# Kernel optimization log

Measured on AMD Instinct MI355X. Metric: run time of the kernel, lower is better.

## Reference

```python
import jax, jax.numpy as jnp
import numpy as np

NUM_HEADS = 32
NUM_KV_HEADS = 8
HEAD_DIM = 64


def rotate_half(x):
    x1, x2 = jnp.split(x, 2, axis=-1)
    return jnp.concatenate((-x2, x1), axis=-1)


def setup_inputs() -> dict:
    key = jax.random.key(0)
    ks = jax.random.split(key, 7)
    B, S, H = 2, 2048, 2048
    hidden_states = jax.random.normal(ks[0], (B, S, H), dtype=jnp.float32)
    # RoPE angles: build realistic cos/sin from inv_freq for positions 0..S-1
    inv_freq = 1.0 / (10000.0 ** (np.arange(0, HEAD_DIM, 2, dtype=np.float32) / HEAD_DIM))
    t = np.arange(S, dtype=np.float32)
    freqs = np.outer(t, inv_freq)  # [S, HEAD_DIM/2]
    emb = np.concatenate([freqs, freqs], axis=-1)  # [S, HEAD_DIM]
    cos = jnp.broadcast_to(jnp.cos(emb)[None], (B, S, HEAD_DIM)).astype(jnp.float32)
    sin = jnp.broadcast_to(jnp.sin(emb)[None], (B, S, HEAD_DIM)).astype(jnp.float32)
    scale = 1.0 / np.sqrt(H)
    Wq = jax.random.normal(ks[1], (NUM_HEADS * HEAD_DIM, H), dtype=jnp.float32) * scale
    Wk = jax.random.normal(ks[2], (NUM_KV_HEADS * HEAD_DIM, H), dtype=jnp.float32) * scale
    Wv = jax.random.normal(ks[3], (NUM_KV_HEADS * HEAD_DIM, H), dtype=jnp.float32) * scale
    Wo = jax.random.normal(ks[4], (H, H), dtype=jnp.float32) * scale
    return {"hidden_states": hidden_states, "cos": cos, "sin": sin,
            "Wq": Wq, "Wk": Wk, "Wv": Wv, "Wo": Wo}


def reference(hidden_states, cos, sin, Wq, Wk, Wv, Wo):
    B, S, H = hidden_states.shape
    hd = HEAD_DIM
    # QKV projections (torch Linear: y = x @ W.T)
    q = jnp.einsum('bsi,oi->bso', hidden_states, Wq).reshape(B, S, NUM_HEADS, hd).transpose(0, 2, 1, 3)
    k = jnp.einsum('bsi,oi->bso', hidden_states, Wk).reshape(B, S, NUM_KV_HEADS, hd).transpose(0, 2, 1, 3)
    v = jnp.einsum('bsi,oi->bso', hidden_states, Wv).reshape(B, S, NUM_KV_HEADS, hd).transpose(0, 2, 1, 3)
    # RoPE: cos/sin [B,S,hd] -> [B,1,S,hd] broadcast over heads
    c = cos[:, None, :, :]
    s = sin[:, None, :, :]
    q = q * c + rotate_half(q) * s
    k = k * c + rotate_half(k) * s
    # GQA: repeat kv heads to match query heads
    groups = NUM_HEADS // NUM_KV_HEADS
    k = jnp.repeat(k, groups, axis=1)
    v = jnp.repeat(v, groups, axis=1)
    scaling = hd ** -0.5
    scores = jnp.einsum('bhqd,bhkd->bhqk', q, k) * scaling
    causal = jnp.tril(jnp.ones((S, S), dtype=bool))
    scores = jnp.where(causal, scores, jnp.finfo(scores.dtype).min)
    attn = jax.nn.softmax(scores, axis=-1)
    y = jnp.einsum('bhqk,bhkd->bhqd', attn, v)
    y = y.transpose(0, 2, 1, 3).reshape(B, S, H)
    return jnp.einsum('bsi,oi->bso', y, Wo)
```

## Files before the change

kernel.cpp:

```cpp
#include <hip/hip_runtime.h>

typedef __bf16 bf16_t;
typedef bf16_t bf16x8 __attribute__((ext_vector_type(8)));
typedef bf16_t bf16x4 __attribute__((ext_vector_type(4)));
typedef float f32x4 __attribute__((ext_vector_type(4)));
typedef float f32x16 __attribute__((ext_vector_type(16)));

#define MFMA16(a, b, c) __builtin_amdgcn_mfma_f32_16x16x32_bf16(a, b, c, 0, 0, 0)
#define MFMA32(a, b, c) __builtin_amdgcn_mfma_f32_32x32x16_bf16(a, b, c, 0, 0, 0)

#define GLOAD16(gsrc, ldst)                                            \
  __builtin_amdgcn_global_load_lds(                                    \
      (const __attribute__((address_space(1))) void*)(gsrc),           \
      (__attribute__((address_space(3))) void*)(ldst), 16, 0, 0)

constexpr int B_ = 2, S_ = 2048, H_ = 2048, NH = 32, NKV = 8, HD = 64;
constexpr int NQKV = NH * HD + 2 * NKV * HD;
constexpr int M_ROWS = B_ * S_;
constexpr float QSCALE = 0.125f * 1.4426950408889634f;

__global__ __launch_bounds__(256) void cvt_kernel(const float* __restrict__ in,
                                                  bf16_t* __restrict__ out, int n8) {
  int i = blockIdx.x * 256 + threadIdx.x;
  if (i >= n8) return;
  const float4* p = (const float4*)(in + (size_t)i * 8);
  float4 a = p[0], b = p[1];
  bf16x8 o;
  o[0] = (bf16_t)a.x; o[1] = (bf16_t)a.y; o[2] = (bf16_t)a.z; o[3] = (bf16_t)a.w;
  o[4] = (bf16_t)b.x; o[5] = (bf16_t)b.y; o[6] = (bf16_t)b.z; o[7] = (bf16_t)b.w;
  *(bf16x8*)(out + (size_t)i * 8) = o;
}

__global__ __launch_bounds__(256) void cvt3_kernel(const float* __restrict__ s0,
                                                   const float* __restrict__ s1,
                                                   const float* __restrict__ s2,
                                                   bf16_t* __restrict__ out) {
  int i = blockIdx.x * 256 + threadIdx.x;
  const float* src;
  long off;
  if (i < 524288) { src = s0; off = i; }
  else if (i < 655360) { src = s1; off = i - 524288; }
  else { src = s2; off = i - 655360; }
  const float4* p = (const float4*)(src + off * 8);
  float4 a = p[0], b = p[1];
  bf16x8 o;
  o[0] = (bf16_t)a.x; o[1] = (bf16_t)a.y; o[2] = (bf16_t)a.z; o[3] = (bf16_t)a.w;
  o[4] = (bf16_t)b.x; o[5] = (bf16_t)b.y; o[6] = (bf16_t)b.z; o[7] = (bf16_t)b.w;
  *(bf16x8*)(out + (size_t)i * 8) = o;
}

template <bool OUT_BF16>
__global__ __launch_bounds__(256) void gemm_bt(const bf16_t* __restrict__ A,
                                               const bf16_t* __restrict__ Bm,
                                               float* __restrict__ Cf,
                                               bf16_t* __restrict__ Cb,
                                               int M, int N, int K) {
  __shared__ __align__(16) bf16_t As[2][128 * 32];
  __shared__ __align__(16) bf16_t Bs[2][128 * 32];
  const int t = threadIdx.x;
  const int lane = t & 63, w = t >> 6;
  const int l15 = lane & 15, l4 = lane >> 4;
  const int wm = w >> 1, wn = w & 1;
  const long Ar0 = (long)blockIdx.y * 128;
  const long Br0 = (long)blockIdx.x * 128;
  const int nt = K >> 5;

  const int scol = ((lane & 3) ^ ((lane >> 3) & 3)) * 8;
  const int srow = lane >> 2;
  auto stage = [&](int kt, int buf) {
#pragma unroll
    for (int c = 0; c < 2; ++c) {
      const int i = w * 2 + c;
      const bf16_t* gA = A + (Ar0 + i * 16 + srow) * (long)K + kt * 32 + scol;
      const bf16_t* gB = Bm + (Br0 + i * 16 + srow) * (long)K + kt * 32 + scol;
      GLOAD16(gA, &As[buf][i * 512]);
      GLOAD16(gB, &Bs[buf][i * 512]);
    }
  };

  f32x4 acc[4][4] = {};
  stage(0, 0);
  __syncthreads();
  int cur = 0;
  const int rsw = l4 ^ ((l15 >> 1) & 3);
  for (int kt = 0; kt < nt; ++kt) {
    if (kt + 1 < nt) stage(kt + 1, cur ^ 1);
    bf16x8 af[4], bfr[4];
#pragma unroll
    for (int mf = 0; mf < 4; ++mf)
      af[mf] = *(const bf16x8*)&As[cur][(wm * 64 + mf * 16 + l15) * 32 + rsw * 8];
#pragma unroll
    for (int nf = 0; nf < 4; ++nf)
      bfr[nf] = *(const bf16x8*)&Bs[cur][(wn * 64 + nf * 16 + l15) * 32 + rsw * 8];
#pragma unroll
    for (int mf = 0; mf < 4; ++mf)
#pragma unroll
      for (int nf = 0; nf < 4; ++nf)
        acc[mf][nf] = MFMA16(af[mf], bfr[nf], acc[mf][nf]);
    __syncthreads();
    cur ^= 1;
  }
#pragma unroll
  for (int mf = 0; mf < 4; ++mf)
#pragma unroll
    for (int nf = 0; nf < 4; ++nf)
#pragma unroll
      for (int r = 0; r < 4; ++r) {
        long row = Ar0 + wm * 64 + mf * 16 + l4 * 4 + r;
        long col = Br0 + wn * 64 + nf * 16 + l15;
        float v = acc[mf][nf][r];
        if (OUT_BF16)
          Cb[row * N + col] = (bf16_t)v;
        else
          Cf[row * N + col] = v;
      }
}

__global__ __launch_bounds__(256) void rope_kernel(bf16_t* __restrict__ qkv,
                                                   const float* __restrict__ cosb,
                                                   const float* __restrict__ sinb) {
  const int head = blockIdx.y;
  const int i = blockIdx.x * 256 + threadIdx.x;
  const long bs = i >> 2;
  const int d0 = (i & 3) * 8;
  const long base = bs * NQKV + (head < 32 ? head * 64 : 2048 + (head - 32) * 64) + d0;
  const float scl = head < 32 ? QSCALE : 1.0f;
  bf16x8 x1 = *(bf16x8*)(qkv + base);
  bf16x8 x2 = *(bf16x8*)(qkv + base + 32);
  const float4* cp = (const float4*)(cosb + bs * 64 + d0);
  const float4* sp = (const float4*)(sinb + bs * 64 + d0);
  const float4 c0 = cp[0], c1 = cp[1];
  const float4 s0 = sp[0], s1 = sp[1];
  const float cc[8] = {c0.x, c0.y, c0.z, c0.w, c1.x, c1.y, c1.z, c1.w};
  const float ss[8] = {s0.x, s0.y, s0.z, s0.w, s1.x, s1.y, s1.z, s1.w};
  bf16x8 y1, y2;
#pragma unroll
  for (int e = 0; e < 8; ++e) {
    const float f1 = (float)x1[e], f2 = (float)x2[e];
    y1[e] = (bf16_t)((f1 * cc[e] - f2 * ss[e]) * scl);
    y2[e] = (bf16_t)((f2 * cc[e] + f1 * ss[e]) * scl);
  }
  *(bf16x8*)(qkv + base) = y1;
  *(bf16x8*)(qkv + base + 32) = y2;
}

__global__ __launch_bounds__(256) void v_transpose(const bf16_t* __restrict__ qkv,
                                                   bf16_t* __restrict__ vT) {
  __shared__ __align__(16) bf16_t lds[64 * 64];
  const int b = blockIdx.z, kvh = blockIdx.y, s0 = blockIdx.x * 64;
  const int t = threadIdx.x;
  auto key = [](int s) { return (((s & 7) ^ ((s >> 3) & 7)) << 3); };
  const int si = t >> 3, j8 = (t & 7) * 8;
  const bf16_t* src = qkv + ((long)(b * S_ + s0 + si)) * NQKV + 2560 + kvh * 64 + j8;
  *(bf16x8*)&lds[si * 64 + (j8 ^ key(si))] = *(const bf16x8*)src;
  *(bf16x8*)&lds[(si + 32) * 64 + (j8 ^ key(si + 32))] =
      *(const bf16x8*)(src + 32L * NQKV);
  __syncthreads();
  const int d = t >> 2, sg = (t & 3) * 16;
  bf16x8 o0, o1;
#pragma unroll
  for (int e = 0; e < 8; ++e) {
    o0[e] = lds[(sg + e) * 64 + (d ^ key(sg + e))];
    o1[e] = lds[(sg + 8 + e) * 64 + (d ^ key(sg + 8 + e))];
  }
  bf16_t* dst = vT + ((long)(b * NKV + kvh) * 64 + d) * S_ + s0 + sg;
  *(bf16x8*)dst = o0;
  *(bf16x8*)(dst + 8) = o1;
}

__device__ __forceinline__ unsigned pkbf16(float lo, float hi) {
  union { bf16_t h[2]; unsigned u; } x;
  x.h[0] = (bf16_t)lo;
  x.h[1] = (bf16_t)hi;
  return x.u;
}

__global__ __launch_bounds__(128) void attn32_kernel(const bf16_t* __restrict__ qkv,
                                                     const bf16_t* __restrict__ vT,
                                                     bf16_t* __restrict__ y) {
  const int h = blockIdx.y;
  const int b = blockIdx.z;
  const int kvh = h >> 2;
  const int t = threadIdx.x, lane = t & 63, w = t >> 6;
  const int l31 = lane & 31, hd = lane >> 5;
  const long bS = (long)b * S_;

  __shared__ __align__(16) bf16_t Klds[2][64 * 64];
  __shared__ __align__(16) bf16_t Vlds[2][64 * 64];

  const bf16_t* kbase = qkv + bS * NQKV + NH * HD + kvh * 64;
  const bf16_t* vbase = vT + ((long)(b * NKV + kvh)) * 64 * S_;

  const int row0 = t >> 3;
  const int slot = t & 7;
  const int wslot8 = ((slot ^ (row0 & 7)) << 3);
  bf16x8 kreg[4], vreg[4];

  auto ldG = [&](int kv0) {
#pragma unroll
    for (int c = 0; c < 4; ++c) {
      kreg[c] = *(const bf16x8*)(kbase + (long)(kv0 + row0 + 16 * c) * NQKV + slot * 8);
      vreg[c] = *(const bf16x8*)(vbase + (long)(row0 + 16 * c) * S_ + kv0 + slot * 8);
    }
  };
  auto wrLDS = [&](int buf) {
#pragma unroll
    for (int c = 0; c < 4; ++c) {
      *(bf16x8*)&Klds[buf][(row0 + 16 * c) * 64 + wslot8] = kreg[c];
      *(bf16x8*)&Vlds[buf][(row0 + 16 * c) * 64 + wslot8] = vreg[c];
    }
  };

  for (int half = 0; half < 2; ++half) {
    const int qt = half ? (int)blockIdx.x : 31 - (int)blockIdx.x;
    const int q0w = qt * 64 + w * 32;
    const int myq = q0w + l31;
    const int NT = qt + 1;

    const bf16_t* qp = qkv + (bS + myq) * NQKV + h * 64 + hd * 8;
    bf16x8 qf[4];
#pragma unroll
    for (int ks = 0; ks < 4; ++ks) qf[ks] = *(const bf16x8*)(qp + ks * 16);

    f32x16 yac[2] = {};
    float m = -1e30f, l = 0.f;

    ldG(0);
    wrLDS(0);
    __syncthreads();

    for (int kt = 0; kt < NT; ++kt) {
      const int buf = kt & 1;
      const int kv0 = kt * 64;
      if (kt + 1 < NT) ldG(kv0 + 64);

      f32x16 sac[2] = {};
      __builtin_amdgcn_s_setprio(1);
#pragma unroll
      for (int ks = 0; ks < 4; ++ks)
#pragma unroll
        for (int kb = 0; kb < 2; ++kb) {
          const int row = kb * 32 + l31;
          const bf16x8 kf =
              *(const bf16x8*)&Klds[buf][row * 64 + (((2 * ks + hd) ^ (row & 7)) << 3)];
          sac[kb] = MFMA32(kf, qf[ks], sac[kb]);
        }
      __builtin_amdgcn_s_setprio(0);
      if (kv0 + 63 > q0w) {
#pragma unroll
        for (int kb = 0; kb < 2; ++kb)
#pragma unroll
          for (int r = 0; r < 16; ++r) {
            const int kv = kv0 + kb * 32 + (r & 3) + 8 * (r >> 2) + 4 * hd;
            if (kv > myq) sac[kb][r] = -3.0e38f;
          }
      }
      float pm4[8], sm4[8];
#pragma unroll
      for (int g = 0; g < 8; ++g) {
        const int kb = g >> 2, r = (g & 3) * 4;
        pm4[g] = fmaxf(fmaxf(sac[kb][r], sac[kb][r + 1]),
                       fmaxf(sac[kb][r + 2], sac[kb][r + 3]));
      }
      float pm = fmaxf(fmaxf(fmaxf(pm4[0], pm4[1]), fmaxf(pm4[2], pm4[3])),
                       fmaxf(fmaxf(pm4[4], pm4[5]), fmaxf(pm4[6], pm4[7])));
      pm = fmaxf(pm, __shfl_xor(pm, 32, 64));
      if (!__all(pm <= m + 8.f)) {
        const float mnew = fmaxf(m, pm);
        const float sc = __builtin_amdgcn_exp2f(m - mnew);
        l *= sc;
        yac[0] *= sc;
        yac[1] *= sc;
        m = mnew;
      }
#pragma unroll
      for (int kb = 0; kb < 2; ++kb)
#pragma unroll
        for (int r = 0; r < 16; ++r)
          sac[kb][r] = __builtin_amdgcn_exp2f(sac[kb][r] - m);
#pragma unroll
      for (int g = 0; g < 8; ++g) {
        const int kb = g >> 2, r = (g & 3) * 4;
        sm4[g] = (sac[kb][r] + sac[kb][r + 1]) + (sac[kb][r + 2] + sac[kb][r + 3]);
      }
      l += ((sm4[0] + sm4[1]) + (sm4[2] + sm4[3])) +
           ((sm4[4] + sm4[5]) + (sm4[6] + sm4[7]));
#pragma unroll
      for (int ks = 0; ks < 4; ++ks) {
        const int kb = ks >> 1;
        const int Bv = 8 * (ks & 1);
        unsigned a0 = pkbf16(sac[kb][Bv + 0], sac[kb][Bv + 1]);
        unsigned b0 = pkbf16(sac[kb][Bv + 4], sac[kb][Bv + 5]);
        unsigned a1 = pkbf16(sac[kb][Bv + 2], sac[kb][Bv + 3]);
        unsigned b1 = pkbf16(sac[kb][Bv + 6], sac[kb][Bv + 7]);
        asm("v_permlane32_swap_b32 %0, %1" : "+v"(a0), "+v"(b0));
        asm("v_permlane32_swap_b32 %0, %1" : "+v"(a1), "+v"(b1));
        union { unsigned u[4]; bf16x8 v; } pu;
        pu.u[0] = a0; pu.u[1] = a1; pu.u[2] = b0; pu.u[3] = b1;
        __builtin_amdgcn_s_setprio(1);
#pragma unroll
        for (int db = 0; db < 2; ++db) {
          const int row = db * 32 + l31;
          const bf16x8 vf =
              *(const bf16x8*)&Vlds[buf][row * 64 + (((2 * ks + hd) ^ (row & 7)) << 3)];
          yac[db] = MFMA32(vf, pu.v, yac[db]);
        }
        __builtin_amdgcn_s_setprio(0);
      }

      if (kt + 1 < NT) wrLDS(buf ^ 1);
      __syncthreads();
    }

    l += __shfl_xor(l, 32, 64);
    const float inv = __builtin_amdgcn_rcpf(l);
    bf16_t* yp = y + (bS + myq) * (long)H_ + h * 64;
#pragma unroll
    for (int db = 0; db < 2; ++db)
#pragma unroll
      for (int g = 0; g < 4; ++g) {
        bf16x4 o;
        o[0] = (bf16_t)(yac[db][4 * g + 0] * inv);
        o[1] = (bf16_t)(yac[db][4 * g + 1] * inv);
        o[2] = (bf16_t)(yac[db][4 * g + 2] * inv);
        o[3] = (bf16_t)(yac[db][4 * g + 3] * inv);
        *(bf16x4*)(yp + db * 32 + 8 * g + 4 * hd) = o;
      }
  }
}

extern "C" void kernel_launch(void* const* d_in, const int* in_sizes, int n_in,
                              void* d_out, int out_size, void* d_ws, size_t ws_size,
                              hipStream_t stream) {
  const float* hs = (const float*)d_in[0];
  const float* cosb = (const float*)d_in[1];
  const float* sinb = (const float*)d_in[2];
  const float* Wq = (const float*)d_in[3];
  const float* Wk = (const float*)d_in[4];
  const float* Wv = (const float*)d_in[5];
  const float* Wo = (const float*)d_in[6];
  float* out = (float*)d_out;

  char* ws = (char*)d_ws;
  bf16_t* hsb  = (bf16_t*)(ws);
  bf16_t* wqkv = (bf16_t*)(ws + 16777216);
  bf16_t* wo   = (bf16_t*)(ws + 29360128);
  bf16_t* qkv  = (bf16_t*)(ws + 37748736);
  bf16_t* vT   = (bf16_t*)(ws + 62914560);
  bf16_t* yb   = (bf16_t*)(ws + 67108864);

  cvt_kernel<<<4096, 256, 0, stream>>>(hs, hsb, 1048576);
  cvt3_kernel<<<3072, 256, 0, stream>>>(Wq, Wk, Wv, wqkv);
  cvt_kernel<<<2048, 256, 0, stream>>>(Wo, wo, 524288);

  gemm_bt<true><<<dim3(24, 32), 256, 0, stream>>>(hsb, wqkv, nullptr, qkv,
                                                  M_ROWS, NQKV, H_);
  rope_kernel<<<dim3(64, 40), 256, 0, stream>>>(qkv, cosb, sinb);
  v_transpose<<<dim3(32, 8, 2), 256, 0, stream>>>(qkv, vT);
  attn32_kernel<<<dim3(16, 32, 2), 128, 0, stream>>>(qkv, vT, yb);
  gemm_bt<false><<<dim3(16, 32), 256, 0, stream>>>(yb, wo, out, nullptr,
                                                   M_ROWS, H_, H_);
}
```

Baseline: 221.6 us.

## Load V fragments directly from global and drop paired-tile blocks in attention

The attention kernel now reads V operands straight from global memory (the transposed V buffer) into registers per lane instead of staging them through LDS. This halves shared memory use and removes the V LDS stores and loads. The grid is doubled so each block handles one query tile rather than a heavy/light pair, with heaviest tiles launched first. The tradeoff is uncoalesced, redundant global V reads per wave (both waves load the same V) and reliance on cache, plus less static load balancing within a block.

```diff
diff --git a/kernel.cpp b/kernel.cpp
--- a/kernel.cpp
+++ b/kernel.cpp
@@ -178,6 +178,7 @@
 __global__ __launch_bounds__(128) void attn32_kernel(const bf16_t* __restrict__ qkv,
                                                      const bf16_t* __restrict__ vT,
                                                      bf16_t* __restrict__ y) {
+  const int qt = 31 - (int)blockIdx.x;
   const int h = blockIdx.y;
   const int b = blockIdx.z;
   const int kvh = h >> 2;
@@ -186,147 +187,154 @@
   const long bS = (long)b * S_;
 
   __shared__ __align__(16) bf16_t Klds[2][64 * 64];
-  __shared__ __align__(16) bf16_t Vlds[2][64 * 64];
 
   const bf16_t* kbase = qkv + bS * NQKV + NH * HD + kvh * 64;
   const bf16_t* vbase = vT + ((long)(b * NKV + kvh)) * 64 * S_;
-
-  const int row0 = t >> 3;
-  const int slot = t & 7;
+  const bf16_t* vlane = vbase + (long)l31 * S_ + hd * 8;
+
+  const int row0 = t >> 3, slot = t & 7;
   const int wslot8 = ((slot ^ (row0 & 7)) << 3);
-  bf16x8 kreg[4], vreg[4];
-
-  auto ldG = [&](int kv0) {
+  const bf16_t* kp[4];
+#pragma unroll
+  for (int c = 0; c < 4; ++c)
+    kp[c] = kbase + (long)(row0 + 16 * c) * NQKV + slot * 8;
+  bf16x8 kreg[4];
+
+  auto ldG = [&]() {
 #pragma unroll
     for (int c = 0; c < 4; ++c) {
-      kreg[c] = *(const bf16x8*)(kbase + (long)(kv0 + row0 + 16 * c) * NQKV + slot * 8);
-      vreg[c] = *(const bf16x8*)(vbase + (long)(row0 + 16 * c) * S_ + kv0 + slot * 8);
+      kreg[c] = *(const bf16x8*)kp[c];
+      kp[c] += 64L * NQKV;
     }
   };
   auto wrLDS = [&](int buf) {
 #pragma unroll
-    for (int c = 0; c < 4; ++c) {
+    for (int c = 0; c < 4; ++c)
       *(bf16x8*)&Klds[buf][(row0 + 16 * c) * 64 + wslot8] = kreg[c];
-      *(bf16x8*)&Vlds[buf][(row0 + 16 * c) * 64 + wslot8] = vreg[c];
-    }
   };
 
-  for (int half = 0; half < 2; ++half) {
-    const int qt = half ? (int)blockIdx.x : 31 - (int)blockIdx.x;
-    const int q0w = qt * 64 + w * 32;
-    const int myq = q0w + l31;
-    const int NT = qt + 1;
-
-    const bf16_t* qp = qkv + (bS + myq) * NQKV + h * 64 + hd * 8;
-    bf16x8 qf[4];
-#pragma unroll
-    for (int ks = 0; ks < 4; ++ks) qf[ks] = *(const bf16x8*)(qp + ks * 16);
-
-    f32x16 yac[2] = {};
-    float m = -1e30f, l = 0.f;
-
-    ldG(0);
-    wrLDS(0);
+  const int q0w = qt * 64 + w * 32;
+  const int myq = q0w + l31;
+  const int NT = qt + 1;
+
+  const bf16_t* qp = qkv + (bS + myq) * NQKV + h * 64 + hd * 8;
+  bf16x8 qf[4];
+#pragma unroll
+  for (int ks = 0; ks < 4; ++ks) qf[ks] = *(const bf16x8*)(qp + ks * 16);
+
+  f32x16 yac[2] = {};
+  float m = -1e30f, l = 0.f;
+
+  ldG();
+  wrLDS(0);
+  __syncthreads();
+
+  for (int kt = 0; kt < NT; ++kt) {
+    const int buf = kt & 1;
+    const int kv0 = kt * 64;
+    if (kt + 1 < NT) ldG();
+
+    const bf16_t* Kb = &Klds[buf][0];
+
+    f32x16 sac[2] = {};
+    __builtin_amdgcn_s_setprio(1);
+#pragma unroll
+    for (int ks = 0; ks < 4; ++ks)
+#pragma unroll
+      for (int kb = 0; kb < 2; ++kb) {
+        const int row = kb * 32 + l31;
+        const bf16x8 kf =
+            *(const bf16x8*)&Kb[row * 64 + (((2 * ks + hd) ^ (row & 7)) << 3)];
+        sac[kb] = MFMA32(kf, qf[ks], sac[kb]);
+      }
+    __builtin_amdgcn_s_setprio(0);
+
+    bf16x8 vld[4][2];
+    {
+      const bf16_t* pv0 = vlane + kv0;
+#pragma unroll
+      for (int ks = 0; ks < 4; ++ks) {
+        vld[ks][0] = *(const bf16x8*)(pv0 + ks * 16);
+        vld[ks][1] = *(const bf16x8*)(pv0 + 32L * S_ + ks * 16);
+      }
+    }
+
+    if (kv0 + 63 > q0w) {
+#pragma unroll
+      for (int kb = 0; kb < 2; ++kb)
+#pragma unroll
+        for (int r = 0; r < 16; ++r) {
+          const int kv = kv0 + kb * 32 + (r & 3) + 8 * (r >> 2) + 4 * hd;
+          if (kv > myq) sac[kb][r] = -3.0e38f;
+        }
+    }
+    float pm4[8], sm4[8];
+#pragma unroll
+    for (int g = 0; g < 8; ++g) {
+      const int kb = g >> 2, r = (g & 3) * 4;
+      pm4[g] = fmaxf(fmaxf(sac[kb][r], sac[kb][r + 1]),
+                     fmaxf(sac[kb][r + 2], sac[kb][r + 3]));
+    }
+    float pm = fmaxf(fmaxf(fmaxf(pm4[0], pm4[1]), fmaxf(pm4[2], pm4[3])),
+                     fmaxf(fmaxf(pm4[4], pm4[5]), fmaxf(pm4[6], pm4[7])));
+    pm = fmaxf(pm, __shfl_xor(pm, 32, 64));
+    if (!__all(pm <= m + 8.f)) {
+      const float mnew = fmaxf(m, pm);
+      const float sc = __builtin_amdgcn_exp2f(m - mnew);
+      l *= sc;
+      yac[0] *= sc;
+      yac[1] *= sc;
+      m = mnew;
+    }
+#pragma unroll
+    for (int kb = 0; kb < 2; ++kb)
+#pragma unroll
+      for (int r = 0; r < 16; ++r)
+        sac[kb][r] = __builtin_amdgcn_exp2f(sac[kb][r] - m);
+#pragma unroll
+    for (int g = 0; g < 8; ++g) {
+      const int kb = g >> 2, r = (g & 3) * 4;
+      sm4[g] = (sac[kb][r] + sac[kb][r + 1]) + (sac[kb][r + 2] + sac[kb][r + 3]);
+    }
+    l += ((sm4[0] + sm4[1]) + (sm4[2] + sm4[3])) +
+         ((sm4[4] + sm4[5]) + (sm4[6] + sm4[7]));
+#pragma unroll
+    for (int ks = 0; ks < 4; ++ks) {
+      const int kb = ks >> 1;
+      const int Bv = 8 * (ks & 1);
+      unsigned a0 = pkbf16(sac[kb][Bv + 0], sac[kb][Bv + 1]);
+      unsigned b0 = pkbf16(sac[kb][Bv + 4], sac[kb][Bv + 5]);
+      unsigned a1 = pkbf16(sac[kb][Bv + 2], sac[kb][Bv + 3]);
+      unsigned b1 = pkbf16(sac[kb][Bv + 6], sac[kb][Bv + 7]);
+      asm("v_permlane32_swap_b32 %0, %1" : "+v"(a0), "+v"(b0));
+      asm("v_permlane32_swap_b32 %0, %1" : "+v"(a1), "+v"(b1));
+      union { unsigned u[4]; bf16x8 v; } pu;
+      pu.u[0] = a0; pu.u[1] = a1; pu.u[2] = b0; pu.u[3] = b1;
+      __builtin_amdgcn_s_setprio(1);
+#pragma unroll
+      for (int db = 0; db < 2; ++db)
+        yac[db] = MFMA32(vld[ks][db], pu.v, yac[db]);
+      __builtin_amdgcn_s_setprio(0);
+    }
+
+    if (kt + 1 < NT) wrLDS(buf ^ 1);
     __syncthreads();
-
-    for (int kt = 0; kt < NT; ++kt) {
-      const int buf = kt & 1;
-      const int kv0 = kt * 64;
-      if (kt + 1 < NT) ldG(kv0 + 64);
-
-      f32x16 sac[2] = {};
-      __builtin_amdgcn_s_setprio(1);
-#pragma unroll
-      for (int ks = 0; ks < 4; ++ks)
-#pragma unroll
-        for (int kb = 0; kb < 2; ++kb) {
-          const int row = kb * 32 + l31;
-          const bf16x8 kf =
-              *(const bf16x8*)&Klds[buf][row * 64 + (((2 * ks + hd) ^ (row & 7)) << 3)];
-          sac[kb] = MFMA32(kf, qf[ks], sac[kb]);
-        }
-      __builtin_amdgcn_s_setprio(0);
-      if (kv0 + 63 > q0w) {
-#pragma unroll
-        for (int kb = 0; kb < 2; ++kb)
-#pragma unroll
-          for (int r = 0; r < 16; ++r) {
-            const int kv = kv0 + kb * 32 + (r & 3) + 8 * (r >> 2) + 4 * hd;
-            if (kv > myq) sac[kb][r] = -3.0e38f;
-          }
-      }
-      float pm4[8], sm4[8];
-#pragma unroll
-      for (int g = 0; g < 8; ++g) {
-        const int kb = g >> 2, r = (g & 3) * 4;
-        pm4[g] = fmaxf(fmaxf(sac[kb][r], sac[kb][r + 1]),
-                       fmaxf(sac[kb][r + 2], sac[kb][r + 3]));
-      }
-      float pm = fmaxf(fmaxf(fmaxf(pm4[0], pm4[1]), fmaxf(pm4[2], pm4[3])),
-                       fmaxf(fmaxf(pm4[4], pm4[5]), fmaxf(pm4[6], pm4[7])));
-      pm = fmaxf(pm, __shfl_xor(pm, 32, 64));
-      if (!__all(pm <= m + 8.f)) {
-        const float mnew = fmaxf(m, pm);
-        const float sc = __builtin_amdgcn_exp2f(m - mnew);
-        l *= sc;
-        yac[0] *= sc;
-        yac[1] *= sc;
-        m = mnew;
-      }
-#pragma unroll
-      for (int kb = 0; kb < 2; ++kb)
-#pragma unroll
-        for (int r = 0; r < 16; ++r)
-          sac[kb][r] = __builtin_amdgcn_exp2f(sac[kb][r] - m);
-#pragma unroll
-      for (int g = 0; g < 8; ++g) {
-        const int kb = g >> 2, r = (g & 3) * 4;
-        sm4[g] = (sac[kb][r] + sac[kb][r + 1]) + (sac[kb][r + 2] + sac[kb][r + 3]);
-      }
-      l += ((sm4[0] + sm4[1]) + (sm4[2] + sm4[3])) +
-           ((sm4[4] + sm4[5]) + (sm4[6] + sm4[7]));
-#pragma unroll
-      for (int ks = 0; ks < 4; ++ks) {
-        const int kb = ks >> 1;
-        const int Bv = 8 * (ks & 1);
-        unsigned a0 = pkbf16(sac[kb][Bv + 0], sac[kb][Bv + 1]);
-        unsigned b0 = pkbf16(sac[kb][Bv + 4], sac[kb][Bv + 5]);
-        unsigned a1 = pkbf16(sac[kb][Bv + 2], sac[kb][Bv + 3]);
-        unsigned b1 = pkbf16(sac[kb][Bv + 6], sac[kb][Bv + 7]);
-        asm("v_permlane32_swap_b32 %0, %1" : "+v"(a0), "+v"(b0));
-        asm("v_permlane32_swap_b32 %0, %1" : "+v"(a1), "+v"(b1));
-        union { unsigned u[4]; bf16x8 v; } pu;
-        pu.u[0] = a0; pu.u[1] = a1; pu.u[2] = b0; pu.u[3] = b1;
-        __builtin_amdgcn_s_setprio(1);
-#pragma unroll
-        for (int db = 0; db < 2; ++db) {
-          const int row = db * 32 + l31;
-          const bf16x8 vf =
-              *(const bf16x8*)&Vlds[buf][row * 64 + (((2 * ks + hd) ^ (row & 7)) << 3)];
-          yac[db] = MFMA32(vf, pu.v, yac[db]);
-        }
-        __builtin_amdgcn_s_setprio(0);
-      }
-
-      if (kt + 1 < NT) wrLDS(buf ^ 1);
-      __syncthreads();
-    }
-
-    l += __shfl_xor(l, 32, 64);
-    const float inv = __builtin_amdgcn_rcpf(l);
-    bf16_t* yp = y + (bS + myq) * (long)H_ + h * 64;
-#pragma unroll
-    for (int db = 0; db < 2; ++db)
-#pragma unroll
-      for (int g = 0; g < 4; ++g) {
-        bf16x4 o;
-        o[0] = (bf16_t)(yac[db][4 * g + 0] * inv);
-        o[1] = (bf16_t)(yac[db][4 * g + 1] * inv);
-        o[2] = (bf16_t)(yac[db][4 * g + 2] * inv);
-        o[3] = (bf16_t)(yac[db][4 * g + 3] * inv);
-        *(bf16x4*)(yp + db * 32 + 8 * g + 4 * hd) = o;
-      }
   }
+
+  l += __shfl_xor(l, 32, 64);
+  const float inv = __builtin_amdgcn_rcpf(l);
+  bf16_t* yp = y + (bS + myq) * (long)H_ + h * 64;
+#pragma unroll
+  for (int db = 0; db < 2; ++db)
+#pragma unroll
+    for (int g = 0; g < 4; ++g) {
+      bf16x4 o;
+      o[0] = (bf16_t)(yac[db][4 * g + 0] * inv);
+      o[1] = (bf16_t)(yac[db][4 * g + 1] * inv);
+      o[2] = (bf16_t)(yac[db][4 * g + 2] * inv);
+      o[3] = (bf16_t)(yac[db][4 * g + 3] * inv);
+      *(bf16x4*)(yp + db * 32 + 8 * g + 4 * hd) = o;
+    }
 }
 
 extern "C" void kernel_launch(void* const* d_in, const int* in_sizes, int n_in,
@@ -357,7 +365,7 @@
                                                   M_ROWS, NQKV, H_);
   rope_kernel<<<dim3(64, 40), 256, 0, stream>>>(qkv, cosb, sinb);
   v_transpose<<<dim3(32, 8, 2), 256, 0, stream>>>(qkv, vT);
-  attn32_kernel<<<dim3(16, 32, 2), 128, 0, stream>>>(qkv, vT, yb);
+  attn32_kernel<<<dim3(32, 32, 2), 128, 0, stream>>>(qkv, vT, yb);
   gemm_bt<false><<<dim3(16, 32), 256, 0, stream>>>(yb, wo, out, nullptr,
                                                    M_ROWS, H_, H_);
 }
```

New measurement: 288.2 us. 1.3x slower.

## Share K/V tiles across the four GQA query heads in one attention block

Applied to the files above, without the earlier changes.

The attention kernel now launches 512 blocks of 512 threads, where each block handles one query tile for all four query heads that share a KV head. The K/V tiles staged in LDS are therefore reused by four heads instead of being loaded once per head. This replaces the earlier two-half loop that paired a long and a short causal tile within one block. Each thread now loads one K and one V vector per tile instead of four. The larger blocks and the launch bound asking for 4 blocks per CU may raise register pressure, and the causal work imbalance between blocks now depends on how the hardware schedules them.

```diff
diff --git a/kernel.cpp b/kernel.cpp
--- a/kernel.cpp
+++ b/kernel.cpp
@@ -175,14 +175,17 @@
   return x.u;
 }
 
-__global__ __launch_bounds__(128) void attn32_kernel(const bf16_t* __restrict__ qkv,
-                                                     const bf16_t* __restrict__ vT,
-                                                     bf16_t* __restrict__ y) {
-  const int h = blockIdx.y;
-  const int b = blockIdx.z;
-  const int kvh = h >> 2;
+__global__ __launch_bounds__(512, 4) void attn32_kernel(const bf16_t* __restrict__ qkv,
+                                                        const bf16_t* __restrict__ vT,
+                                                        bf16_t* __restrict__ y) {
+  const int bx = blockIdx.x;
+  const int p = (bx >> 1) & 15;
+  const int qt = (bx & 1) ? p : 31 - p;
+  const int kvh = (bx >> 5) & 7;
+  const int b = bx >> 8;
   const int t = threadIdx.x, lane = t & 63, w = t >> 6;
   const int l31 = lane & 31, hd = lane >> 5;
+  const int h = kvh * 4 + (w >> 1);
   const long bS = (long)b * S_;
 
   __shared__ __align__(16) bf16_t Klds[2][64 * 64];
@@ -191,142 +194,139 @@
   const bf16_t* kbase = qkv + bS * NQKV + NH * HD + kvh * 64;
   const bf16_t* vbase = vT + ((long)(b * NKV + kvh)) * 64 * S_;
 
-  const int row0 = t >> 3;
-  const int slot = t & 7;
+  const int row0 = t >> 3, slot = t & 7;
   const int wslot8 = ((slot ^ (row0 & 7)) << 3);
-  bf16x8 kreg[4], vreg[4];
-
-  auto ldG = [&](int kv0) {
-#pragma unroll
-    for (int c = 0; c < 4; ++c) {
-      kreg[c] = *(const bf16x8*)(kbase + (long)(kv0 + row0 + 16 * c) * NQKV + slot * 8);
-      vreg[c] = *(const bf16x8*)(vbase + (long)(row0 + 16 * c) * S_ + kv0 + slot * 8);
-    }
+  const bf16_t* kp = kbase + (long)row0 * NQKV + slot * 8;
+  const bf16_t* vp = vbase + (long)row0 * S_ + slot * 8;
+  bf16x8 kreg, vreg;
+
+  auto ldG = [&]() {
+    kreg = *(const bf16x8*)kp;
+    vreg = *(const bf16x8*)vp;
+    kp += 64L * NQKV;
+    vp += 64;
   };
   auto wrLDS = [&](int buf) {
-#pragma unroll
-    for (int c = 0; c < 4; ++c) {
-      *(bf16x8*)&Klds[buf][(row0 + 16 * c) * 64 + wslot8] = kreg[c];
-      *(bf16x8*)&Vlds[buf][(row0 + 16 * c) * 64 + wslot8] = vreg[c];
-    }
+    *(bf16x8*)&Klds[buf][row0 * 64 + wslot8] = kreg;
+    *(bf16x8*)&Vlds[buf][row0 * 64 + wslot8] = vreg;
   };
 
-  for (int half = 0; half < 2; ++half) {
-    const int qt = half ? (int)blockIdx.x : 31 - (int)blockIdx.x;
-    const int q0w = qt * 64 + w * 32;
-    const int myq = q0w + l31;
-    const int NT = qt + 1;
-
-    const bf16_t* qp = qkv + (bS + myq) * NQKV + h * 64 + hd * 8;
-    bf16x8 qf[4];
-#pragma unroll
-    for (int ks = 0; ks < 4; ++ks) qf[ks] = *(const bf16x8*)(qp + ks * 16);
-
-    f32x16 yac[2] = {};
-    float m = -1e30f, l = 0.f;
-
-    ldG(0);
-    wrLDS(0);
+  const int q0w = qt * 64 + (w & 1) * 32;
+  const int myq = q0w + l31;
+  const int NT = qt + 1;
+
+  const bf16_t* qp = qkv + (bS + myq) * NQKV + h * 64 + hd * 8;
+  bf16x8 qf[4];
+#pragma unroll
+  for (int ks = 0; ks < 4; ++ks) qf[ks] = *(const bf16x8*)(qp + ks * 16);
+
+  f32x16 yac[2] = {};
+  float m = -1e30f, l = 0.f;
+
+  ldG();
+  wrLDS(0);
+  __syncthreads();
+
+  for (int kt = 0; kt < NT; ++kt) {
+    const int buf = kt & 1;
+    const int kv0 = kt * 64;
+    if (kt + 1 < NT) ldG();
+
+    const bf16_t* Kb = &Klds[buf][0];
+    const bf16_t* Vb = &Vlds[buf][0];
+
+    f32x16 sac[2] = {};
+    __builtin_amdgcn_s_setprio(1);
+#pragma unroll
+    for (int ks = 0; ks < 4; ++ks)
+#pragma unroll
+      for (int kb = 0; kb < 2; ++kb) {
+        const int row = kb * 32 + l31;
+        const bf16x8 kf =
+            *(const bf16x8*)&Kb[row * 64 + (((2 * ks + hd) ^ (row & 7)) << 3)];
+        sac[kb] = MFMA32(kf, qf[ks], sac[kb]);
+      }
+    __builtin_amdgcn_s_setprio(0);
+    if (kv0 + 63 > q0w) {
+#pragma unroll
+      for (int kb = 0; kb < 2; ++kb)
+#pragma unroll
+        for (int r = 0; r < 16; ++r) {
+          const int kv = kv0 + kb * 32 + (r & 3) + 8 * (r >> 2) + 4 * hd;
+          if (kv > myq) sac[kb][r] = -3.0e38f;
+        }
+    }
+    float pm4[8], sm4[8];
+#pragma unroll
+    for (int g = 0; g < 8; ++g) {
+      const int kb = g >> 2, r = (g & 3) * 4;
+      pm4[g] = fmaxf(fmaxf(sac[kb][r], sac[kb][r + 1]),
+                     fmaxf(sac[kb][r + 2], sac[kb][r + 3]));
+    }
+    float pm = fmaxf(fmaxf(fmaxf(pm4[0], pm4[1]), fmaxf(pm4[2], pm4[3])),
+                     fmaxf(fmaxf(pm4[4], pm4[5]), fmaxf(pm4[6], pm4[7])));
+    pm = fmaxf(pm, __shfl_xor(pm, 32, 64));
+    if (!__all(pm <= m + 8.f)) {
+      const float mnew = fmaxf(m, pm);
+      const float sc = __builtin_amdgcn_exp2f(m - mnew);
+      l *= sc;
+      yac[0] *= sc;
+      yac[1] *= sc;
+      m = mnew;
+    }
+#pragma unroll
+    for (int kb = 0; kb < 2; ++kb)
+#pragma unroll
+      for (int r = 0; r < 16; ++r)
+        sac[kb][r] = __builtin_amdgcn_exp2f(sac[kb][r] - m);
+#pragma unroll
+    for (int g = 0; g < 8; ++g) {
+      const int kb = g >> 2, r = (g & 3) * 4;
+      sm4[g] = (sac[kb][r] + sac[kb][r + 1]) + (sac[kb][r + 2] + sac[kb][r + 3]);
+    }
+    l += ((sm4[0] + sm4[1]) + (sm4[2] + sm4[3])) +
+         ((sm4[4] + sm4[5]) + (sm4[6] + sm4[7]));
+#pragma unroll
+    for (int ks = 0; ks < 4; ++ks) {
+      const int kb = ks >> 1;
+      const int Bv = 8 * (ks & 1);
+      unsigned a0 = pkbf16(sac[kb][Bv + 0], sac[kb][Bv + 1]);
+      unsigned b0 = pkbf16(sac[kb][Bv + 4], sac[kb][Bv + 5]);
+      unsigned a1 = pkbf16(sac[kb][Bv + 2], sac[kb][Bv + 3]);
+      unsigned b1 = pkbf16(sac[kb][Bv + 6], sac[kb][Bv + 7]);
+      asm("v_permlane32_swap_b32 %0, %1" : "+v"(a0), "+v"(b0));
+      asm("v_permlane32_swap_b32 %0, %1" : "+v"(a1), "+v"(b1));
+      union { unsigned u[4]; bf16x8 v; } pu;
+      pu.u[0] = a0; pu.u[1] = a1; pu.u[2] = b0; pu.u[3] = b1;
+      __builtin_amdgcn_s_setprio(1);
+#pragma unroll
+      for (int db = 0; db < 2; ++db) {
+        const int row = db * 32 + l31;
+        const bf16x8 vf =
+            *(const bf16x8*)&Vb[row * 64 + (((2 * ks + hd) ^ (row & 7)) << 3)];
+        yac[db] = MFMA32(vf, pu.v, yac[db]);
+      }
+      __builtin_amdgcn_s_setprio(0);
+    }
+
+    if (kt + 1 < NT) wrLDS(buf ^ 1);
     __syncthreads();
-
-    for (int kt = 0; kt < NT; ++kt) {
-      const int buf = kt & 1;
-      const int kv0 = kt * 64;
-      if (kt + 1 < NT) ldG(kv0 + 64);
-
-      f32x16 sac[2] = {};
-      __builtin_amdgcn_s_setprio(1);
-#pragma unroll
-      for (int ks = 0; ks < 4; ++ks)
-#pragma unroll
-        for (int kb = 0; kb < 2; ++kb) {
-          const int row = kb * 32 + l31;
-          const bf16x8 kf =
-              *(const bf16x8*)&Klds[buf][row * 64 + (((2 * ks + hd) ^ (row & 7)) << 3)];
-          sac[kb] = MFMA32(kf, qf[ks], sac[kb]);
-        }
-      __builtin_amdgcn_s_setprio(0);
-      if (kv0 + 63 > q0w) {
-#pragma unroll
-        for (int kb = 0; kb < 2; ++kb)
-#pragma unroll
-          for (int r = 0; r < 16; ++r) {
-            const int kv = kv0 + kb * 32 + (r & 3) + 8 * (r >> 2) + 4 * hd;
-            if (kv > myq) sac[kb][r] = -3.0e38f;
-          }
-      }
-      float pm4[8], sm4[8];
-#pragma unroll
-      for (int g = 0; g < 8; ++g) {
-        const int kb = g >> 2, r = (g & 3) * 4;
-        pm4[g] = fmaxf(fmaxf(sac[kb][r], sac[kb][r + 1]),
-                       fmaxf(sac[kb][r + 2], sac[kb][r + 3]));
-      }
-      float pm = fmaxf(fmaxf(fmaxf(pm4[0], pm4[1]), fmaxf(pm4[2], pm4[3])),
-                       fmaxf(fmaxf(pm4[4], pm4[5]), fmaxf(pm4[6], pm4[7])));
-      pm = fmaxf(pm, __shfl_xor(pm, 32, 64));
-      if (!__all(pm <= m + 8.f)) {
-        const float mnew = fmaxf(m, pm);
-        const float sc = __builtin_amdgcn_exp2f(m - mnew);
-        l *= sc;
-        yac[0] *= sc;
-        yac[1] *= sc;
-        m = mnew;
-      }
-#pragma unroll
-      for (int kb = 0; kb < 2; ++kb)
-#pragma unroll
-        for (int r = 0; r < 16; ++r)
-          sac[kb][r] = __builtin_amdgcn_exp2f(sac[kb][r] - m);
-#pragma unroll
-      for (int g = 0; g < 8; ++g) {
-        const int kb = g >> 2, r = (g & 3) * 4;
-        sm4[g] = (sac[kb][r] + sac[kb][r + 1]) + (sac[kb][r + 2] + sac[kb][r + 3]);
-      }
-      l += ((sm4[0] + sm4[1]) + (sm4[2] + sm4[3])) +
-           ((sm4[4] + sm4[5]) + (sm4[6] + sm4[7]));
-#pragma unroll
-      for (int ks = 0; ks < 4; ++ks) {
-        const int kb = ks >> 1;
-        const int Bv = 8 * (ks & 1);
-        unsigned a0 = pkbf16(sac[kb][Bv + 0], sac[kb][Bv + 1]);
-        unsigned b0 = pkbf16(sac[kb][Bv + 4], sac[kb][Bv + 5]);
-        unsigned a1 = pkbf16(sac[kb][Bv + 2], sac[kb][Bv + 3]);
-        unsigned b1 = pkbf16(sac[kb][Bv + 6], sac[kb][Bv + 7]);
-        asm("v_permlane32_swap_b32 %0, %1" : "+v"(a0), "+v"(b0));
-        asm("v_permlane32_swap_b32 %0, %1" : "+v"(a1), "+v"(b1));
-        union { unsigned u[4]; bf16x8 v; } pu;
-        pu.u[0] = a0; pu.u[1] = a1; pu.u[2] = b0; pu.u[3] = b1;
-        __builtin_amdgcn_s_setprio(1);
-#pragma unroll
-        for (int db = 0; db < 2; ++db) {
-          const int row = db * 32 + l31;
-          const bf16x8 vf =
-              *(const bf16x8*)&Vlds[buf][row * 64 + (((2 * ks + hd) ^ (row & 7)) << 3)];
-          yac[db] = MFMA32(vf, pu.v, yac[db]);
-        }
-        __builtin_amdgcn_s_setprio(0);
-      }
-
-      if (kt + 1 < NT) wrLDS(buf ^ 1);
-      __syncthreads();
-    }
-
-    l += __shfl_xor(l, 32, 64);
-    const float inv = __builtin_amdgcn_rcpf(l);
-    bf16_t* yp = y + (bS + myq) * (long)H_ + h * 64;
-#pragma unroll
-    for (int db = 0; db < 2; ++db)
-#pragma unroll
-      for (int g = 0; g < 4; ++g) {
-        bf16x4 o;
-        o[0] = (bf16_t)(yac[db][4 * g + 0] * inv);
-        o[1] = (bf16_t)(yac[db][4 * g + 1] * inv);
-        o[2] = (bf16_t)(yac[db][4 * g + 2] * inv);
-        o[3] = (bf16_t)(yac[db][4 * g + 3] * inv);
-        *(bf16x4*)(yp + db * 32 + 8 * g + 4 * hd) = o;
-      }
   }
+
+  l += __shfl_xor(l, 32, 64);
+  const float inv = __builtin_amdgcn_rcpf(l);
+  bf16_t* yp = y + (bS + myq) * (long)H_ + h * 64;
+#pragma unroll
+  for (int db = 0; db < 2; ++db)
+#pragma unroll
+    for (int g = 0; g < 4; ++g) {
+      bf16x4 o;
+      o[0] = (bf16_t)(yac[db][4 * g + 0] * inv);
+      o[1] = (bf16_t)(yac[db][4 * g + 1] * inv);
+      o[2] = (bf16_t)(yac[db][4 * g + 2] * inv);
+      o[3] = (bf16_t)(yac[db][4 * g + 3] * inv);
+      *(bf16x4*)(yp + db * 32 + 8 * g + 4 * hd) = o;
+    }
 }
 
 extern "C" void kernel_launch(void* const* d_in, const int* in_sizes, int n_in,
@@ -357,7 +357,7 @@
                                                   M_ROWS, NQKV, H_);
   rope_kernel<<<dim3(64, 40), 256, 0, stream>>>(qkv, cosb, sinb);
   v_transpose<<<dim3(32, 8, 2), 256, 0, stream>>>(qkv, vT);
-  attn32_kernel<<<dim3(16, 32, 2), 128, 0, stream>>>(qkv, vT, yb);
+  attn32_kernel<<<512, 512, 0, stream>>>(qkv, vT, yb);
   gemm_bt<false><<<dim3(16, 32), 256, 0, stream>>>(yb, wo, out, nullptr,
                                                    M_ROWS, H_, H_);
 }
```

Measured after the change: 229.8 us. 1.04x slower.
